# Kernel tuning notes

Measured on AMD Instinct MI355X. Metric: run time of the kernel, lower is better.

## Reference

```python
import jax, jax.numpy as jnp
import numpy as np

B, T, V, C, D = 32, 512, 25, 64, 128
EPS = 1e-5


def _shift_indices(num_nodes, ch, sign):
    i = np.arange(num_nodes)[:, None]
    j = np.arange(ch)[None, :]
    idx = (i * ch + j + sign * j * ch) % (ch * num_nodes)
    return jnp.asarray(idx.reshape(-1).astype(np.int32))


def setup_inputs() -> dict:
    key = jax.random.key(0)
    ks = jax.random.split(key, 6)
    return {
        "x0": jax.random.normal(ks[0], (B, T, V, C), jnp.float32),
        "feature_mask": jax.random.normal(ks[1], (1, V, C), jnp.float32) * 0.1,
        "W": jax.random.normal(ks[2], (C, D), jnp.float32) * (1.0 / np.sqrt(D)),
        "lin_b": jax.random.normal(ks[3], (1, 1, D), jnp.float32) * 0.02,
        "bn_gamma": jnp.ones((V * D,), jnp.float32),
        "bn_beta": jnp.zeros((V * D,), jnp.float32),
        "down_w": jax.random.normal(ks[4], (D, C), jnp.float32) * (1.0 / np.sqrt(C)),
        "down_b": jax.random.normal(ks[5], (D,), jnp.float32) * 0.02,
        "dbn_gamma": jnp.ones((D,), jnp.float32),
        "dbn_beta": jnp.zeros((D,), jnp.float32),
        "shift_in": _shift_indices(V, C, +1),
        "shift_out": _shift_indices(V, D, -1),
    }


def reference(x0, feature_mask, W, lin_b, bn_gamma, bn_beta,
              down_w, down_b, dbn_gamma, dbn_beta, shift_in, shift_out):
    b, t, v, c = x0.shape
    d = W.shape[1]
    n = b * t
    # shift-in gather over flattened (V*C) feature axis
    x = x0.reshape(n, v * c)[:, shift_in].reshape(n, v, c)
    # learned feature mask
    x = x * (jnp.tanh(feature_mask) + 1.0)
    # small per-node linear
    x = jnp.einsum('nvc,cd->nvd', x, W) + lin_b
    # shift-out gather
    x = x.reshape(n, v * d)[:, shift_out]
    # BatchNorm1d (training-mode batch stats, biased variance)
    mu = x.mean(0)
    var = x.var(0)
    x = (x - mu) * (bn_gamma / jnp.sqrt(var + EPS)) + bn_beta
    x = x.reshape(b, t, v, d).transpose(0, 3, 1, 2)  # (B, D, T, V)
    # residual down path: 1x1 conv == per-position matmul, then BN2d
    res = jnp.einsum('btvc,dc->btvd', x0, down_w) + down_b
    rmu = res.mean((0, 1, 2))
    rvar = res.var((0, 1, 2))
    res = (res - rmu) * (dbn_gamma / jnp.sqrt(rvar + EPS)) + dbn_beta
    res = res.transpose(0, 3, 1, 2)  # (B, D, T, V)
    return jax.nn.relu(x + res)
```

## Files before the change

kernel.cpp:

```cpp
#include <hip/hip_runtime.h>

#define VV 25
#define CC 64
#define DD 128
#define NN 16384
#define NVS 409600
#define VC 1600
#define VD 3200
#define EPSF 1e-5f

#define WS_MASK   0
#define WS_WPACK  1600
#define WS_DWPACK 5696
#define WS_ABY    9792
#define WS_ABR    16192
#define WS_COLSUM 16448
#define WS_QY     18048
#define WS_QR     21248

typedef __attribute__((ext_vector_type(8))) short s16x8;
typedef __attribute__((ext_vector_type(4))) short s16x4;
typedef __attribute__((ext_vector_type(4))) float f32x4;

__device__ __forceinline__ short f2bf(float f) {
  unsigned u = __builtin_bit_cast(unsigned, f);
  u += 0x7fffu + ((u >> 16) & 1u);
  return (short)(u >> 16);
}
__device__ __forceinline__ float bf2f(short s) {
  unsigned u = ((unsigned)(unsigned short)s) << 16;
  return __builtin_bit_cast(float, u);
}

__global__ void k_init(const float* __restrict__ fm, const float* __restrict__ W,
                       const float* __restrict__ dw, float* __restrict__ ws) {
  int g = blockIdx.x * 256 + threadIdx.x;
  if (g < VC) ws[WS_MASK + g] = tanhf(fm[g]) + 1.0f;
  if (g < 4928) ws[WS_COLSUM + g] = 0.0f;
  if (g >= 2048 && g < 3072) {
    int idx = g - 2048;
    int frag = idx >> 6, lane = idx & 63;
    int nt = frag >> 1, k = frag & 1, q = lane >> 4, l = lane & 15;
    s16x8 pk;
#pragma unroll
    for (int j = 0; j < 8; j++) {
      int c = k * 32 + q * 8 + j;
      pk[j] = f2bf(W[c * DD + nt * 16 + l]);
    }
    ((s16x8*)(ws + WS_WPACK))[idx] = pk;
  }
  if (g >= 3072 && g < 4096) {
    int idx = g - 3072;
    int frag = idx >> 6, lane = idx & 63;
    int nt = frag >> 1, k = frag & 1, q = lane >> 4, l = lane & 15;
    s16x8 pk;
#pragma unroll
    for (int j = 0; j < 8; j++) {
      int c = k * 32 + q * 8 + j;
      pk[j] = f2bf(dw[(nt * 16 + l) * CC + c]);
    }
    ((s16x8*)(ws + WS_DWPACK))[idx] = pk;
  }
}

__launch_bounds__(256, 2)
__global__ void k_stats(const float* __restrict__ x0, float* __restrict__ ws) {
  __shared__ short s_raw[200 * 72];
  __shared__ short s_xm[200 * 72];
  __shared__ short s_zero[96];
  __shared__ float s_col[1600];
  __shared__ float s_qy[3200];
  int tid = threadIdx.x;
  int wave = tid >> 6, lane = tid & 63, quad = lane >> 4, l15 = lane & 15;
  for (int t = tid; t < 96; t += 256) s_zero[t] = 0;
  for (int t = tid; t < 1600; t += 256) s_col[t] = 0.0f;
  for (int t = tid; t < 3200; t += 256) s_qy[t] = 0.0f;
  const s16x8* wpack = (const s16x8*)(ws + WS_WPACK);
  const s16x8* dwpack = (const s16x8*)(ws + WS_DWPACK);
  const float* mask = ws + WS_MASK;

  int nt0 = wave * 2;
  s16x8 bw[2][2], bd[2][2];
#pragma unroll
  for (int a = 0; a < 2; a++) {
    int nt = nt0 + a;
    bw[a][0] = wpack[(nt * 2 + 0) * 64 + lane];
    bw[a][1] = wpack[(nt * 2 + 1) * 64 + lane];
    bd[a][0] = dwpack[(nt * 2 + 0) * 64 + lane];
    bd[a][1] = dwpack[(nt * 2 + 1) * 64 + lane];
  }
  float rq[2] = {0.f, 0.f};

  for (int chunk = 0; chunk < 4; chunk++) {
    int n0 = blockIdx.x * 32 + chunk * 8;
    __syncthreads();
    for (int t = tid; t < 3200; t += 256) {
      int flat = t * 4;
      const float4 xv = *(const float4*)(x0 + (size_t)n0 * VC + flat);
      int nl = flat / VC;
      int j = flat - nl * VC;
      int v = j >> 6, c = j & 63;
      s16x4 pk; pk[0]=f2bf(xv.x); pk[1]=f2bf(xv.y); pk[2]=f2bf(xv.z); pk[3]=f2bf(xv.w);
      *(s16x4*)(s_raw + (v * 8 + nl) * 72 + c) = pk;
      atomicAdd(&s_col[j + 0], xv.x);
      atomicAdd(&s_col[j + 1], xv.y);
      atomicAdd(&s_col[j + 2], xv.z);
      atomicAdd(&s_col[j + 3], xv.w);
    }
    __syncthreads();
    for (int t = tid; t < 3200; t += 256) {
      int flat = t * 4;
      int nl = flat / VC;
      int f = flat - nl * VC;
      int v = f >> 6, c = f & 63;
      const float4 mk = *(const float4*)(mask + f);
      float mka[4] = {mk.x, mk.y, mk.z, mk.w};
      s16x4 pk;
#pragma unroll
      for (int jj = 0; jj < 4; jj++) {
        int cc = c + jj;
        int p = (f + jj + (cc << 6)) % VC;
        float xv = bf2f(s_raw[((p >> 6) * 8 + nl) * 72 + (p & 63)]);
        pk[jj] = f2bf(xv * mka[jj]);
      }
      *(s16x4*)(s_xm + (v * 8 + nl) * 72 + c) = pk;
    }
    __syncthreads();
#pragma unroll 1
    for (int v = 0; v < 25; v++) {
      const short* bx = (l15 < 8) ? (const short*)(s_xm + (v * 8 + l15) * 72) : (const short*)s_zero;
      const short* br = (l15 < 8) ? (const short*)(s_raw + (v * 8 + l15) * 72) : (const short*)s_zero;
      s16x8 a0 = *(const s16x8*)(bx + quad * 8);
      s16x8 a1 = *(const s16x8*)(bx + 32 + quad * 8);
      s16x8 r0 = *(const s16x8*)(br + quad * 8);
      s16x8 r1 = *(const s16x8*)(br + 32 + quad * 8);
#pragma unroll
      for (int a = 0; a < 2; a++) {
        f32x4 acc = {0.f, 0.f, 0.f, 0.f};
        acc = __builtin_amdgcn_mfma_f32_16x16x32_bf16(a0, bw[a][0], acc, 0, 0, 0);
        acc = __builtin_amdgcn_mfma_f32_16x16x32_bf16(a1, bw[a][1], acc, 0, 0, 0);
        float q = acc[0]*acc[0] + acc[1]*acc[1] + acc[2]*acc[2] + acc[3]*acc[3];
        q += __shfl_xor(q, 16, 64); q += __shfl_xor(q, 32, 64);
        if (quad == 0) atomicAdd(&s_qy[v * 128 + (nt0 + a) * 16 + l15], q);
        f32x4 rc = {0.f, 0.f, 0.f, 0.f};
        rc = __builtin_amdgcn_mfma_f32_16x16x32_bf16(r0, bd[a][0], rc, 0, 0, 0);
        rc = __builtin_amdgcn_mfma_f32_16x16x32_bf16(r1, bd[a][1], rc, 0, 0, 0);
        rq[a] += rc[0]*rc[0] + rc[1]*rc[1] + rc[2]*rc[2] + rc[3]*rc[3];
      }
    }
  }
  __syncthreads();
  for (int t = tid; t < 1600; t += 256) atomicAdd(ws + WS_COLSUM + t, s_col[t]);
  for (int t = tid; t < 3200; t += 256) atomicAdd(ws + WS_QY + t, s_qy[t]);
#pragma unroll
  for (int a = 0; a < 2; a++) {
    float q = rq[a];
    q += __shfl_xor(q, 16, 64); q += __shfl_xor(q, 32, 64);
    if (quad == 0) atomicAdd(ws + WS_QR + (nt0 + a) * 16 + l15, q);
  }
}

__global__ void k_reduce(const float* __restrict__ gamma, const float* __restrict__ beta,
                         const float* __restrict__ dgamma, const float* __restrict__ dbeta,
                         const float* __restrict__ W, const float* __restrict__ dw,
                         float* __restrict__ ws) {
  if (blockIdx.x == 25) {
    __shared__ float s_cs[64];
    int t = threadIdx.x;
    if (t < 64) {
      float s = 0.f;
#pragma unroll
      for (int v = 0; v < 25; v++) s += ws[WS_COLSUM + v * 64 + t];
      s_cs[t] = s;
    }
    __syncthreads();
    int d = t;
    float m = 0.f;
#pragma unroll 8
    for (int c = 0; c < 64; c++) m += s_cs[c] * dw[d * 64 + c];
    m *= (1.0f / 409600.0f);
    float q = ws[WS_QR + d] * (1.0f / 409600.0f);
    float var = q - m * m;
    float rs = rsqrtf(var + EPSF);
    float a = dgamma[d] * rs;
    ((float2*)(ws + WS_ABR))[d] = make_float2(a, dbeta[d] - m * a);
    return;
  }
  int f = blockIdx.x * 128 + threadIdx.x;
  int v = f >> 7, d = f & 127;
  float m = 0.f;
#pragma unroll 8
  for (int c = 0; c < 64; c++) {
    int p = (v * 64 + 65 * c) % VC;
    m += ws[WS_COLSUM + p] * ws[WS_MASK + v * 64 + c] * W[c * DD + d];
  }
  m *= (1.0f / 16384.0f);
  float q = ws[WS_QY + f] * (1.0f / 16384.0f);
  float var = q - m * m;
  float rs = rsqrtf(var + EPSF);
  int vo = v + d % 25; if (vo >= 25) vo -= 25;
  int j = vo * 128 + d;
  float a = gamma[j] * rs;
  ((float2*)(ws + WS_ABY))[f] = make_float2(a, beta[j] - m * a);
}

__launch_bounds__(256, 2)
__global__ void k_main(const float* __restrict__ x0, const float* __restrict__ ws,
                       float* __restrict__ out) {
  __shared__ short s_raw[112 * 72];
  __shared__ short s_xm[112 * 72];
  __shared__ short s_ybuf[100 * 129];
  int tid = threadIdx.x;
  int wave = tid >> 6, lane = tid & 63, quad = lane >> 4, l15 = lane & 15;
  int n0 = blockIdx.x * 4;
  const float* mask = ws + WS_MASK;
  for (int t = tid; t < 1600; t += 256) {
    int flat = t * 4;
    const float4 xv = *(const float4*)(x0 + (size_t)n0 * VC + flat);
    int nl = flat / VC;
    int j = flat - nl * VC;
    int v = j >> 6, c = j & 63;
    s16x4 pk; pk[0]=f2bf(xv.x); pk[1]=f2bf(xv.y); pk[2]=f2bf(xv.z); pk[3]=f2bf(xv.w);
    *(s16x4*)(s_raw + (nl * 25 + v) * 72 + c) = pk;
  }
  __syncthreads();
  for (int t = tid; t < 1600; t += 256) {
    int flat = t * 4;
    int nl = flat / VC;
    int f = flat - nl * VC;
    int v = f >> 6, c = f & 63;
    const float4 mk = *(const float4*)(mask + f);
    float mka[4] = {mk.x, mk.y, mk.z, mk.w};
    s16x4 pk;
#pragma unroll
    for (int jj = 0; jj < 4; jj++) {
      int cc = c + jj;
      int p = (f + jj + (cc << 6)) % VC;
      float xv = bf2f(s_raw[(nl * 25 + (p >> 6)) * 72 + (p & 63)]);
      pk[jj] = f2bf(xv * mka[jj]);
    }
    *(s16x4*)(s_xm + (nl * 25 + v) * 72 + c) = pk;
  }
  __syncthreads();
  const s16x8* wpack = (const s16x8*)(ws + WS_WPACK);
  const float2* aby = (const float2*)(ws + WS_ABY);
  {
    s16x8 b0, b1;
#pragma unroll
    for (int ji = 0; ji < 14; ji++) {
      int job = wave * 14 + ji;
      int nt = job / 7, mt = job - nt * 7;
      if (ji == 0 || ji == 7) {
        b0 = wpack[(nt * 2 + 0) * 64 + lane];
        b1 = wpack[(nt * 2 + 1) * 64 + lane];
      }
      int mbase = mt * 16;
      const short* pa = s_xm + (mbase + l15) * 72 + quad * 8;
      s16x8 a0 = *(const s16x8*)(pa);
      s16x8 a1 = *(const s16x8*)(pa + 32);
      f32x4 acc = {0.f, 0.f, 0.f, 0.f};
      acc = __builtin_amdgcn_mfma_f32_16x16x32_bf16(a0, b0, acc, 0, 0, 0);
      acc = __builtin_amdgcn_mfma_f32_16x16x32_bf16(a1, b1, acc, 0, 0, 0);
      int d = nt * 16 + l15;
      int d25 = d % 25;
#pragma unroll
      for (int i = 0; i < 4; i++) {
        int s = mbase + quad * 4 + i;
        if (s < 100) {
          int r = s / 25;
          int vv = s - r * 25;
          float2 ab = aby[vv * 128 + d];
          float val = acc[i] * ab.x + ab.y;
          int vo = vv + d25; if (vo >= 25) vo -= 25;
          s_ybuf[(r * 25 + vo) * 129 + d] = f2bf(val);
        }
      }
    }
  }
  __syncthreads();
  const s16x8* dwpack = (const s16x8*)(ws + WS_DWPACK);
  const float2* abr = (const float2*)(ws + WS_ABR);
  {
    s16x8 b0, b1; float2 ab = make_float2(0.f, 0.f);
#pragma unroll
    for (int ji = 0; ji < 14; ji++) {
      int job = wave * 14 + ji;
      int nt = job / 7, mt = job - nt * 7;
      if (ji == 0 || ji == 7) {
        b0 = dwpack[(nt * 2 + 0) * 64 + lane];
        b1 = dwpack[(nt * 2 + 1) * 64 + lane];
        ab = abr[nt * 16 + l15];
      }
      int mbase = mt * 16;
      const short* pa = s_raw + (mbase + l15) * 72 + quad * 8;
      s16x8 a0 = *(const s16x8*)(pa);
      s16x8 a1 = *(const s16x8*)(pa + 32);
      f32x4 acc = {0.f, 0.f, 0.f, 0.f};
      acc = __builtin_amdgcn_mfma_f32_16x16x32_bf16(a0, b0, acc, 0, 0, 0);
      acc = __builtin_amdgcn_mfma_f32_16x16x32_bf16(a1, b1, acc, 0, 0, 0);
      int d = nt * 16 + l15;
#pragma unroll
      for (int i = 0; i < 4; i++) {
        int s = mbase + quad * 4 + i;
        if (s < 100) {
          int r = s / 25;
          int vv = s - r * 25;
          int ad = (r * 25 + vv) * 129 + d;
          float val = acc[i] * ab.x + ab.y + bf2f(s_ybuf[ad]);
          val = fmaxf(val, 0.0f);
          s_ybuf[ad] = f2bf(val);
        }
      }
    }
  }
  __syncthreads();
  int b = n0 >> 9, t0 = n0 & 511;
  float* ob = out + (size_t)b * 1638400 + (size_t)t0 * 25;
  for (int idx = tid; idx < 12800; idx += 256) {
    int dd = idx / 100;
    int q = idx - dd * 100;
    ob[(size_t)dd * 12800 + q] = bf2f(s_ybuf[q * 129 + dd]);
  }
}

extern "C" void kernel_launch(void* const* d_in, const int* in_sizes, int n_in,
                              void* d_out, int out_size, void* d_ws, size_t ws_size,
                              hipStream_t stream) {
  const float* x0    = (const float*)d_in[0];
  const float* fm    = (const float*)d_in[1];
  const float* W     = (const float*)d_in[2];
  const float* bn_g  = (const float*)d_in[4];
  const float* bn_b  = (const float*)d_in[5];
  const float* dw    = (const float*)d_in[6];
  const float* dbn_g = (const float*)d_in[8];
  const float* dbn_b = (const float*)d_in[9];
  float* ws = (float*)d_ws;
  float* out = (float*)d_out;
  k_init<<<20, 256, 0, stream>>>(fm, W, dw, ws);
  k_stats<<<512, 256, 0, stream>>>(x0, ws);
  k_reduce<<<26, 128, 0, stream>>>(bn_g, bn_b, dbn_g, dbn_b, W, dw, ws);
  k_main<<<4096, 256, 0, stream>>>(x0, ws, out);
}
```

Measured before the change: 643.4 us.

## Fuse shift-gather into staging, drop LDS atomics, write per-block stat partials

```diff
diff --git a/kernel.cpp b/kernel.cpp
--- a/kernel.cpp
+++ b/kernel.cpp
@@ -1,22 +1,16 @@
 #include <hip/hip_runtime.h>
 
-#define VV 25
-#define CC 64
-#define DD 128
-#define NN 16384
-#define NVS 409600
 #define VC 1600
-#define VD 3200
 #define EPSF 1e-5f
 
-#define WS_MASK   0
+#define WS_MASKJ  0
 #define WS_WPACK  1600
 #define WS_DWPACK 5696
 #define WS_ABY    9792
 #define WS_ABR    16192
 #define WS_COLSUM 16448
-#define WS_QY     18048
-#define WS_QR     21248
+#define WS_QYP    18048
+#define QYP_STRIDE 3328
 
 typedef __attribute__((ext_vector_type(8))) short s16x8;
 typedef __attribute__((ext_vector_type(4))) short s16x4;
@@ -32,11 +26,29 @@
   return __builtin_bit_cast(float, u);
 }
 
+__device__ __forceinline__ void stage_elem(int j, int base, int vstr, float4 xv,
+                                           const float* mj, short* s_raw, short* s_xm) {
+  int u = j >> 6, c = j & 63;
+  s16x4 pk; pk[0]=f2bf(xv.x); pk[1]=f2bf(xv.y); pk[2]=f2bf(xv.z); pk[3]=f2bf(xv.w);
+  *(s16x4*)(s_raw + (base + u*vstr)*72 + c) = pk;
+  int v0 = (u - c + 75) % 25;
+  float xa[4] = {xv.x, xv.y, xv.z, xv.w};
+#pragma unroll
+  for (int e = 0; e < 4; e++) {
+    int ve = v0 - e; if (ve < 0) ve += 25;
+    s_xm[(base + ve*vstr)*72 + c + e] = f2bf(xa[e] * mj[e]);
+  }
+}
+
 __global__ void k_init(const float* __restrict__ fm, const float* __restrict__ W,
                        const float* __restrict__ dw, float* __restrict__ ws) {
   int g = blockIdx.x * 256 + threadIdx.x;
-  if (g < VC) ws[WS_MASK + g] = tanhf(fm[g]) + 1.0f;
-  if (g < 4928) ws[WS_COLSUM + g] = 0.0f;
+  if (g < VC) {
+    int c = g & 63, jv = g >> 6;
+    int v = (jv - c + 75) % 25;
+    ws[WS_MASKJ + g] = tanhf(fm[v * 64 + c]) + 1.0f;
+    ws[WS_COLSUM + g] = 0.0f;
+  }
   if (g >= 2048 && g < 3072) {
     int idx = g - 2048;
     int frag = idx >> 6, lane = idx & 63;
@@ -45,7 +57,7 @@
 #pragma unroll
     for (int j = 0; j < 8; j++) {
       int c = k * 32 + q * 8 + j;
-      pk[j] = f2bf(W[c * DD + nt * 16 + l]);
+      pk[j] = f2bf(W[c * 128 + nt * 16 + l]);
     }
     ((s16x8*)(ws + WS_WPACK))[idx] = pk;
   }
@@ -57,7 +69,7 @@
 #pragma unroll
     for (int j = 0; j < 8; j++) {
       int c = k * 32 + q * 8 + j;
-      pk[j] = f2bf(dw[(nt * 16 + l) * CC + c]);
+      pk[j] = f2bf(dw[(nt * 16 + l) * 64 + c]);
     }
     ((s16x8*)(ws + WS_DWPACK))[idx] = pk;
   }
@@ -65,19 +77,15 @@
 
 __launch_bounds__(256, 2)
 __global__ void k_stats(const float* __restrict__ x0, float* __restrict__ ws) {
-  __shared__ short s_raw[200 * 72];
-  __shared__ short s_xm[200 * 72];
-  __shared__ short s_zero[96];
-  __shared__ float s_col[1600];
-  __shared__ float s_qy[3200];
+  __shared__ short s_raw[14976];
+  __shared__ short s_xm[14976];
+  __shared__ float s_qy[3328];
   int tid = threadIdx.x;
   int wave = tid >> 6, lane = tid & 63, quad = lane >> 4, l15 = lane & 15;
-  for (int t = tid; t < 96; t += 256) s_zero[t] = 0;
-  for (int t = tid; t < 1600; t += 256) s_col[t] = 0.0f;
-  for (int t = tid; t < 3200; t += 256) s_qy[t] = 0.0f;
+  for (int t = tid; t < 3328; t += 256) s_qy[t] = 0.f;
+  for (int t = tid; t < 576; t += 256) { s_raw[14400 + t] = 0; s_xm[14400 + t] = 0; }
   const s16x8* wpack = (const s16x8*)(ws + WS_WPACK);
   const s16x8* dwpack = (const s16x8*)(ws + WS_DWPACK);
-  const float* mask = ws + WS_MASK;
 
   int nt0 = wave * 2;
   s16x8 bw[2][2], bd[2][2];
@@ -89,74 +97,69 @@
     bd[a][0] = dwpack[(nt * 2 + 0) * 64 + lane];
     bd[a][1] = dwpack[(nt * 2 + 1) * 64 + lane];
   }
-  float rq[2] = {0.f, 0.f};
+  float mj0[4], mj1[4];
+  {
+    float4 m4 = *(const float4*)(ws + WS_MASKJ + tid * 4);
+    mj0[0]=m4.x; mj0[1]=m4.y; mj0[2]=m4.z; mj0[3]=m4.w;
+  }
+  if (tid < 144) {
+    float4 m4 = *(const float4*)(ws + WS_MASKJ + 1024 + tid * 4);
+    mj1[0]=m4.x; mj1[1]=m4.y; mj1[2]=m4.z; mj1[3]=m4.w;
+  }
+  float cs[8] = {0,0,0,0,0,0,0,0};
+  float rq0 = 0.f, rq1 = 0.f;
 
   for (int chunk = 0; chunk < 4; chunk++) {
     int n0 = blockIdx.x * 32 + chunk * 8;
     __syncthreads();
-    for (int t = tid; t < 3200; t += 256) {
-      int flat = t * 4;
-      const float4 xv = *(const float4*)(x0 + (size_t)n0 * VC + flat);
-      int nl = flat / VC;
-      int j = flat - nl * VC;
-      int v = j >> 6, c = j & 63;
-      s16x4 pk; pk[0]=f2bf(xv.x); pk[1]=f2bf(xv.y); pk[2]=f2bf(xv.z); pk[3]=f2bf(xv.w);
-      *(s16x4*)(s_raw + (v * 8 + nl) * 72 + c) = pk;
-      atomicAdd(&s_col[j + 0], xv.x);
-      atomicAdd(&s_col[j + 1], xv.y);
-      atomicAdd(&s_col[j + 2], xv.z);
-      atomicAdd(&s_col[j + 3], xv.w);
-    }
-    __syncthreads();
-    for (int t = tid; t < 3200; t += 256) {
-      int flat = t * 4;
-      int nl = flat / VC;
-      int f = flat - nl * VC;
-      int v = f >> 6, c = f & 63;
-      const float4 mk = *(const float4*)(mask + f);
-      float mka[4] = {mk.x, mk.y, mk.z, mk.w};
-      s16x4 pk;
-#pragma unroll
-      for (int jj = 0; jj < 4; jj++) {
-        int cc = c + jj;
-        int p = (f + jj + (cc << 6)) % VC;
-        float xv = bf2f(s_raw[((p >> 6) * 8 + nl) * 72 + (p & 63)]);
-        pk[jj] = f2bf(xv * mka[jj]);
-      }
-      *(s16x4*)(s_xm + (v * 8 + nl) * 72 + c) = pk;
+    for (int r = 0; r < 8; r++) {
+      const float* rowp = x0 + (size_t)(n0 + r) * VC;
+      float4 xv = *(const float4*)(rowp + tid * 4);
+      cs[0]+=xv.x; cs[1]+=xv.y; cs[2]+=xv.z; cs[3]+=xv.w;
+      stage_elem(tid * 4, r, 8, xv, mj0, s_raw, s_xm);
+      if (tid < 144) {
+        float4 xw = *(const float4*)(rowp + 1024 + tid * 4);
+        cs[4]+=xw.x; cs[5]+=xw.y; cs[6]+=xw.z; cs[7]+=xw.w;
+        stage_elem(1024 + tid * 4, r, 8, xw, mj1, s_raw, s_xm);
+      }
     }
     __syncthreads();
 #pragma unroll 1
-    for (int v = 0; v < 25; v++) {
-      const short* bx = (l15 < 8) ? (const short*)(s_xm + (v * 8 + l15) * 72) : (const short*)s_zero;
-      const short* br = (l15 < 8) ? (const short*)(s_raw + (v * 8 + l15) * 72) : (const short*)s_zero;
-      s16x8 a0 = *(const s16x8*)(bx + quad * 8);
-      s16x8 a1 = *(const s16x8*)(bx + 32 + quad * 8);
-      s16x8 r0 = *(const s16x8*)(br + quad * 8);
-      s16x8 r1 = *(const s16x8*)(br + 32 + quad * 8);
+    for (int vp = 0; vp < 13; vp++) {
+      int rb = vp * 16;
+      const short* px = s_xm + (rb + l15) * 72 + quad * 8;
+      const short* pr = s_raw + (rb + l15) * 72 + quad * 8;
+      s16x8 a0 = *(const s16x8*)px;
+      s16x8 a1 = *(const s16x8*)(px + 32);
+      s16x8 r0 = *(const s16x8*)pr;
+      s16x8 r1 = *(const s16x8*)(pr + 32);
+      int vq = vp * 2 + (quad >> 1);
 #pragma unroll
       for (int a = 0; a < 2; a++) {
         f32x4 acc = {0.f, 0.f, 0.f, 0.f};
         acc = __builtin_amdgcn_mfma_f32_16x16x32_bf16(a0, bw[a][0], acc, 0, 0, 0);
         acc = __builtin_amdgcn_mfma_f32_16x16x32_bf16(a1, bw[a][1], acc, 0, 0, 0);
         float q = acc[0]*acc[0] + acc[1]*acc[1] + acc[2]*acc[2] + acc[3]*acc[3];
-        q += __shfl_xor(q, 16, 64); q += __shfl_xor(q, 32, 64);
-        if (quad == 0) atomicAdd(&s_qy[v * 128 + (nt0 + a) * 16 + l15], q);
+        atomicAdd(&s_qy[vq * 128 + (nt0 + a) * 16 + l15], q);
         f32x4 rc = {0.f, 0.f, 0.f, 0.f};
         rc = __builtin_amdgcn_mfma_f32_16x16x32_bf16(r0, bd[a][0], rc, 0, 0, 0);
         rc = __builtin_amdgcn_mfma_f32_16x16x32_bf16(r1, bd[a][1], rc, 0, 0, 0);
-        rq[a] += rc[0]*rc[0] + rc[1]*rc[1] + rc[2]*rc[2] + rc[3]*rc[3];
-      }
-    }
-  }
-  __syncthreads();
-  for (int t = tid; t < 1600; t += 256) atomicAdd(ws + WS_COLSUM + t, s_col[t]);
-  for (int t = tid; t < 3200; t += 256) atomicAdd(ws + WS_QY + t, s_qy[t]);
-#pragma unroll
-  for (int a = 0; a < 2; a++) {
-    float q = rq[a];
-    q += __shfl_xor(q, 16, 64); q += __shfl_xor(q, 32, 64);
-    if (quad == 0) atomicAdd(ws + WS_QR + (nt0 + a) * 16 + l15, q);
+        float t2 = rc[0]*rc[0] + rc[1]*rc[1] + rc[2]*rc[2] + rc[3]*rc[3];
+        if (a == 0) rq0 += t2; else rq1 += t2;
+      }
+    }
+  }
+  __syncthreads();
+  atomicAdd(&s_qy[3200 + nt0 * 16 + l15], rq0);
+  atomicAdd(&s_qy[3200 + (nt0 + 1) * 16 + l15], rq1);
+  __syncthreads();
+  float* qp = ws + WS_QYP + (size_t)blockIdx.x * QYP_STRIDE;
+  for (int t = tid; t < 3328; t += 256) qp[t] = s_qy[t];
+#pragma unroll
+  for (int e = 0; e < 4; e++) atomicAdd(ws + WS_COLSUM + tid * 4 + e, cs[e]);
+  if (tid < 144) {
+#pragma unroll
+    for (int e = 0; e < 4; e++) atomicAdd(ws + WS_COLSUM + 1024 + tid * 4 + e, cs[4 + e]);
   }
 }
 
@@ -164,44 +167,52 @@
                          const float* __restrict__ dgamma, const float* __restrict__ dbeta,
                          const float* __restrict__ W, const float* __restrict__ dw,
                          float* __restrict__ ws) {
+  int tid = threadIdx.x;
   if (blockIdx.x == 25) {
     __shared__ float s_cs[64];
-    int t = threadIdx.x;
-    if (t < 64) {
+    if (tid < 64) {
       float s = 0.f;
 #pragma unroll
-      for (int v = 0; v < 25; v++) s += ws[WS_COLSUM + v * 64 + t];
-      s_cs[t] = s;
+      for (int v = 0; v < 25; v++) s += ws[WS_COLSUM + v * 64 + tid];
+      s_cs[tid] = s;
     }
     __syncthreads();
-    int d = t;
+    int d = tid;
+    float q = 0.f;
+#pragma unroll 8
+    for (int b2 = 0; b2 < 512; b2++) q += ws[WS_QYP + (size_t)b2 * QYP_STRIDE + 3200 + d];
     float m = 0.f;
 #pragma unroll 8
     for (int c = 0; c < 64; c++) m += s_cs[c] * dw[d * 64 + c];
     m *= (1.0f / 409600.0f);
-    float q = ws[WS_QR + d] * (1.0f / 409600.0f);
-    float var = q - m * m;
-    float rs = rsqrtf(var + EPSF);
-    float a = dgamma[d] * rs;
+    float var = q * (1.0f / 409600.0f) - m * m;
+    float a = dgamma[d] * rsqrtf(var + EPSF);
     ((float2*)(ws + WS_ABR))[d] = make_float2(a, dbeta[d] - m * a);
     return;
   }
-  int f = blockIdx.x * 128 + threadIdx.x;
+  __shared__ float s_cm[1600];
+  for (int t = tid; t < 1600; t += 128)
+    s_cm[t] = ws[WS_COLSUM + t] * ws[WS_MASKJ + t];
+  __syncthreads();
+  int f = blockIdx.x * 128 + tid;
   int v = f >> 7, d = f & 127;
+  float q = 0.f;
+#pragma unroll 8
+  for (int b2 = 0; b2 < 512; b2++) q += ws[WS_QYP + (size_t)b2 * QYP_STRIDE + f];
   float m = 0.f;
+  int p = v * 64;
 #pragma unroll 8
   for (int c = 0; c < 64; c++) {
-    int p = (v * 64 + 65 * c) % VC;
-    m += ws[WS_COLSUM + p] * ws[WS_MASK + v * 64 + c] * W[c * DD + d];
+    m += s_cm[p] * W[c * 128 + d];
+    p += 65; if (p >= VC) p -= VC;
   }
   m *= (1.0f / 16384.0f);
-  float q = ws[WS_QY + f] * (1.0f / 16384.0f);
-  float var = q - m * m;
-  float rs = rsqrtf(var + EPSF);
-  int vo = v + d % 25; if (vo >= 25) vo -= 25;
-  int j = vo * 128 + d;
-  float a = gamma[j] * rs;
-  ((float2*)(ws + WS_ABY))[f] = make_float2(a, beta[j] - m * a);
+  float var = q * (1.0f / 16384.0f) - m * m;
+  int d25 = d % 25;
+  int vo = v + d25; if (vo >= 25) vo -= 25;
+  int jg = vo * 128 + d;
+  float a = gamma[jg] * rsqrtf(var + EPSF);
+  ((float2*)(ws + WS_ABY))[f] = make_float2(a, beta[jg] - m * a);
 }
 
 __launch_bounds__(256, 2)
@@ -213,33 +224,14 @@
   int tid = threadIdx.x;
   int wave = tid >> 6, lane = tid & 63, quad = lane >> 4, l15 = lane & 15;
   int n0 = blockIdx.x * 4;
-  const float* mask = ws + WS_MASK;
-  for (int t = tid; t < 1600; t += 256) {
-    int flat = t * 4;
-    const float4 xv = *(const float4*)(x0 + (size_t)n0 * VC + flat);
-    int nl = flat / VC;
-    int j = flat - nl * VC;
-    int v = j >> 6, c = j & 63;
-    s16x4 pk; pk[0]=f2bf(xv.x); pk[1]=f2bf(xv.y); pk[2]=f2bf(xv.z); pk[3]=f2bf(xv.w);
-    *(s16x4*)(s_raw + (nl * 25 + v) * 72 + c) = pk;
-  }
-  __syncthreads();
   for (int t = tid; t < 1600; t += 256) {
     int flat = t * 4;
     int nl = flat / VC;
-    int f = flat - nl * VC;
-    int v = f >> 6, c = f & 63;
-    const float4 mk = *(const float4*)(mask + f);
-    float mka[4] = {mk.x, mk.y, mk.z, mk.w};
-    s16x4 pk;
-#pragma unroll
-    for (int jj = 0; jj < 4; jj++) {
-      int cc = c + jj;
-      int p = (f + jj + (cc << 6)) % VC;
-      float xv = bf2f(s_raw[(nl * 25 + (p >> 6)) * 72 + (p & 63)]);
-      pk[jj] = f2bf(xv * mka[jj]);
-    }
-    *(s16x4*)(s_xm + (nl * 25 + v) * 72 + c) = pk;
+    int j = flat - nl * VC;
+    float4 xv = *(const float4*)(x0 + (size_t)n0 * VC + flat);
+    float4 m4 = *(const float4*)(ws + WS_MASKJ + j);
+    float mj[4] = {m4.x, m4.y, m4.z, m4.w};
+    stage_elem(j, nl * 25, 1, xv, mj, s_raw, s_xm);
   }
   __syncthreads();
   const s16x8* wpack = (const s16x8*)(ws + WS_WPACK);
@@ -316,10 +308,16 @@
   __syncthreads();
   int b = n0 >> 9, t0 = n0 & 511;
   float* ob = out + (size_t)b * 1638400 + (size_t)t0 * 25;
-  for (int idx = tid; idx < 12800; idx += 256) {
-    int dd = idx / 100;
-    int q = idx - dd * 100;
-    ob[(size_t)dd * 12800 + q] = bf2f(s_ybuf[q * 129 + dd]);
+  for (int it = tid; it < 3200; it += 256) {
+    int dd = it / 25;
+    int qg = it - dd * 25;
+    int q0 = qg * 4;
+    float4 o;
+    o.x = bf2f(s_ybuf[(q0 + 0) * 129 + dd]);
+    o.y = bf2f(s_ybuf[(q0 + 1) * 129 + dd]);
+    o.z = bf2f(s_ybuf[(q0 + 2) * 129 + dd]);
+    o.w = bf2f(s_ybuf[(q0 + 3) * 129 + dd]);
+    *(float4*)(ob + (size_t)dd * 12800 + q0) = o;
   }
 }
 
```

After: 617.8 us. -4.0%, faster.
